# Optimization experiments

Hardware: AMD Instinct MI355X
Metric: run time of the kernel (lower is better)

Reference implementation:

```python
import jax, jax.numpy as jnp
import numpy as np

N_NODES = 50000
N_EDGES = 800000
IN_FEATS = 64
HID_FEATS = 64


def _sage_conv(x, src, dst, W_self, W_neigh, b):
    # mean aggregation over in-neighbors (messages flow src -> dst)
    msg_sum = jax.ops.segment_sum(x[src], dst, num_segments=N_NODES)  # [N, d]
    deg = jax.ops.segment_sum(jnp.ones((src.shape[0],), x.dtype), dst,
                              num_segments=N_NODES)  # [N]
    h_neigh = msg_sum / jnp.maximum(deg, 1.0)[:, None]  # zero-degree nodes -> 0
    return x @ W_self + h_neigh @ W_neigh + b


def setup_inputs() -> dict:
    key = jax.random.key(0)
    ks = jax.random.split(key, 12)
    inputs = jax.random.normal(ks[0], (N_NODES, IN_FEATS), dtype=jnp.float32)
    src = jax.random.randint(ks[1], (N_EDGES,), 0, N_NODES, dtype=jnp.int32)
    dst = jax.random.randint(ks[2], (N_EDGES,), 0, N_NODES, dtype=jnp.int32)

    def glorot(k, shape):
        lim = float(np.sqrt(6.0 / (shape[0] + shape[1])))
        return jax.random.uniform(k, shape, jnp.float32, -lim, lim)

    return {
        "inputs": inputs, "src": src, "dst": dst,
        "W_self1": glorot(ks[3], (IN_FEATS, HID_FEATS)),
        "W_neigh1": glorot(ks[4], (IN_FEATS, HID_FEATS)),
        "b1": jnp.zeros((HID_FEATS,), jnp.float32),
        "W_self2": glorot(ks[5], (HID_FEATS, HID_FEATS)),
        "W_neigh2": glorot(ks[6], (HID_FEATS, HID_FEATS)),
        "b2": jnp.zeros((HID_FEATS,), jnp.float32),
        "W_self3": glorot(ks[7], (HID_FEATS, 1)),
        "W_neigh3": glorot(ks[8], (HID_FEATS, 1)),
        "b3": jnp.zeros((1,), jnp.float32),
    }


def reference(inputs, src, dst,
              W_self1, W_neigh1, b1,
              W_self2, W_neigh2, b2,
              W_self3, W_neigh3, b3):
    h = jax.nn.relu(_sage_conv(inputs, src, dst, W_self1, W_neigh1, b1))
    h = jax.nn.relu(_sage_conv(h, src, dst, W_self2, W_neigh2, b2))
    h = _sage_conv(h, src, dst, W_self3, W_neigh3, b3)
    return h  # [N_NODES, 1]
```

## Files before the change

kernel.cpp:

```cpp
#include <hip/hip_runtime.h>

#define N_NODES 50000
#define N_EDGES 800000
#define F 64
#define NTILES (N_NODES / 16)

#define BNODES 128
#define NB ((N_NODES + BNODES - 1) / BNODES)
#define BCAP 2560
#define EPB 3200
#define SCAT_BLOCKS (N_EDGES / EPB)
#define PREP_ELEMS (4 * F * F + N_NODES * 16)
#define PREP_BLOCKS ((PREP_ELEMS + 511) / 512)

typedef __attribute__((ext_vector_type(8))) short short8;
typedef __attribute__((ext_vector_type(4))) float f32x4;

union frag16 { uint4 u; short8 s; };


__device__ __forceinline__ float bflo(unsigned int u) {
    union { unsigned int i; float f; } c; c.i = u << 16; return c.f;
}
__device__ __forceinline__ float bfhi(unsigned int u) {
    union { unsigned int i; float f; } c; c.i = u & 0xFFFF0000u; return c.f;
}
__device__ __forceinline__ unsigned short f2bf(float f) {
    union { float f; unsigned int i; } c; c.f = f;
    unsigned int r = c.i + 0x7FFF + ((c.i >> 16) & 1);
    return (unsigned short)(r >> 16);
}


__global__ __launch_bounds__(512) void scatter_prep(
        const int* __restrict__ src, const int* __restrict__ dst,
        int* __restrict__ bcur, unsigned int* __restrict__ binned,
        const float* __restrict__ W0, const float* __restrict__ W1,
        const float* __restrict__ W2, const float* __restrict__ W3,
        unsigned short* __restrict__ Wt,
        const float4* __restrict__ xin, ushort4* __restrict__ xout) {
    if (blockIdx.x >= SCAT_BLOCKS) {
        int idx = (blockIdx.x - SCAT_BLOCKS) * 512 + threadIdx.x;
        if (idx < 4 * F * F) {
            int m = idx >> 12;
            int e = idx & 4095;
            int n = e >> 6, k = e & 63;
            const float* W = (m == 0) ? W0 : (m == 1) ? W1 : (m == 2) ? W2 : W3;
            Wt[m * F * F + n * F + k] = f2bf(W[k * F + n]);
            return;
        }
        int i = idx - 4 * F * F;
        if (i >= N_NODES * 16) return;
        float4 v = xin[i];
        ushort4 o;
        o.x = f2bf(v.x); o.y = f2bf(v.y); o.z = f2bf(v.z); o.w = f2bf(v.w);
        xout[i] = o;
        return;
    }

    __shared__ int lcnt[NB];
    __shared__ int scan[512];
    __shared__ int gbase[NB];
    __shared__ int lcur[NB];
    __shared__ unsigned int staged[EPB];
    int tid = threadIdx.x;
    int e0 = blockIdx.x * EPB;
    int e1 = min(N_EDGES, e0 + EPB);
    for (int i = tid; i < NB; i += 512) lcnt[i] = 0;
    __syncthreads();
    for (int i = e0 + tid; i < e1; i += 512)
        atomicAdd(&lcnt[dst[i] >> 7], 1);
    __syncthreads();
    int v = (tid < NB) ? lcnt[tid] : 0;
    scan[tid] = v;
    __syncthreads();
    for (int off = 1; off < 512; off <<= 1) {
        int t = (tid >= off) ? scan[tid - off] : 0;
        __syncthreads();
        scan[tid] += t;
        __syncthreads();
    }
    if (tid < NB) {
        int excl = scan[tid] - v;
        int resv = (v > 0) ? atomicAdd(&bcur[tid], v) : 0;
        gbase[tid] = tid * BCAP + resv - excl;
        lcur[tid] = excl;
    }
    __syncthreads();
    for (int i = e0 + tid; i < e1; i += 512) {
        int d = dst[i];
        int b = d >> 7;
        int dl = d & 127;
        int posl = atomicAdd(&lcur[b], 1);
        staged[posl] = (unsigned)src[i] | ((unsigned)dl << 16) | ((unsigned)b << 23);
    }
    __syncthreads();
    int cnt = e1 - e0;
    for (int i = tid; i < cnt; i += 512) {
        unsigned pk = staged[i];
        int b = pk >> 23;
        binned[gbase[b] + i] = pk;
    }
}


__global__ __launch_bounds__(256) void bucket_build(const unsigned int* __restrict__ binned,
                                                    const int* __restrict__ bcur,
                                                    int* __restrict__ row_beg,
                                                    unsigned short* __restrict__ degs,
                                                    unsigned short* __restrict__ csr16) {
    int b = blockIdx.x;
    int start = b * BCAP;
    int cnt = bcur[b];
    __shared__ int ncnt[BNODES];
    __shared__ int nofs[BNODES];
    __shared__ int ncur[BNODES];
    int tid = threadIdx.x;
    for (int i = tid; i < BNODES; i += 256) ncnt[i] = 0;
    __syncthreads();
    for (int i = tid; i < cnt; i += 256)
        atomicAdd(&ncnt[(binned[start + i] >> 16) & 127], 1);
    __syncthreads();
    if (tid < 128) nofs[tid] = ncnt[tid];
    __syncthreads();
    for (int off = 1; off < 128; off <<= 1) {
        int t = (tid >= off && tid < 128) ? nofs[tid - off] : 0;
        __syncthreads();
        if (tid < 128) nofs[tid] += t;
        __syncthreads();
    }
    if (tid < 128) {
        int excl = nofs[tid] - ncnt[tid];
        ncur[tid] = excl;
        int node = b * BNODES + tid;
        row_beg[node] = start + excl;
        degs[node] = (unsigned short)ncnt[tid];
    }
    __syncthreads();
    for (int i = tid; i < cnt; i += 256) {
        unsigned pk = binned[start + i];
        int dl = (pk >> 16) & 127;
        int pos = start + atomicAdd(&ncur[dl], 1);
        csr16[pos] = (unsigned short)(pk & 0xFFFF);
    }
}


__global__ __launch_bounds__(256) void aggregate_kernel(
        const uint4* __restrict__ xh8, const int* __restrict__ row_beg,
        const unsigned short* __restrict__ degs,
        const unsigned short* __restrict__ csr16, uint4* __restrict__ aggh8, int n_nodes) {
    int wave = threadIdx.x >> 6;
    int lane = threadIdx.x & 63;
    int node = blockIdx.x * 4 + wave;
    if (node >= n_nodes) return;
    int g   = lane >> 3;
    int sub = lane & 7;
    int beg = row_beg[node];
    int deg = degs[node];
    int end = beg + deg;
    float a0[8], a1[8];
    #pragma unroll
    for (int j = 0; j < 8; ++j) { a0[j] = 0.f; a1[j] = 0.f; }
    int i = beg + g;
    for (; i + 8 < end; i += 16) {
        int i0 = csr16[i];
        int i1 = csr16[i + 8];
        uint4 v0 = xh8[i0 * 8 + sub];
        uint4 v1 = xh8[i1 * 8 + sub];
        a0[0] += bflo(v0.x); a0[1] += bfhi(v0.x); a0[2] += bflo(v0.y); a0[3] += bfhi(v0.y);
        a0[4] += bflo(v0.z); a0[5] += bfhi(v0.z); a0[6] += bflo(v0.w); a0[7] += bfhi(v0.w);
        a1[0] += bflo(v1.x); a1[1] += bfhi(v1.x); a1[2] += bflo(v1.y); a1[3] += bfhi(v1.y);
        a1[4] += bflo(v1.z); a1[5] += bfhi(v1.z); a1[6] += bflo(v1.w); a1[7] += bfhi(v1.w);
    }
    if (i < end) {
        uint4 v0 = xh8[csr16[i] * 8 + sub];
        a0[0] += bflo(v0.x); a0[1] += bfhi(v0.x); a0[2] += bflo(v0.y); a0[3] += bfhi(v0.y);
        a0[4] += bflo(v0.z); a0[5] += bfhi(v0.z); a0[6] += bflo(v0.w); a0[7] += bfhi(v0.w);
    }
    float s[8];
    #pragma unroll
    for (int j = 0; j < 8; ++j) s[j] = a0[j] + a1[j];
    #pragma unroll
    for (int off = 8; off <= 32; off <<= 1)
        #pragma unroll
        for (int j = 0; j < 8; ++j)
            s[j] += __shfl_xor(s[j], off);
    if (g == 0) {
        float inv = (deg > 0) ? (1.0f / (float)deg) : 0.f;
        unsigned short o[8];
        #pragma unroll
        for (int j = 0; j < 8; ++j) o[j] = f2bf(s[j] * inv);
        uint4 pk;
        pk.x = (unsigned)o[0] | ((unsigned)o[1] << 16);
        pk.y = (unsigned)o[2] | ((unsigned)o[3] << 16);
        pk.z = (unsigned)o[4] | ((unsigned)o[5] << 16);
        pk.w = (unsigned)o[6] | ((unsigned)o[7] << 16);
        aggh8[node * 8 + sub] = pk;
    }
}


__global__ __launch_bounds__(256) void mfma_transform(
        const uint4* __restrict__ xh, const uint4* __restrict__ aggh,
        const uint4* __restrict__ Wst, const uint4* __restrict__ Wnt,
        const float* __restrict__ b,
        unsigned short* __restrict__ out_bf,
        const float* __restrict__ Ws3, const float* __restrict__ Wn3,
        float* __restrict__ pout, float* __restrict__ qout, int ntiles) {
    int wv   = threadIdx.x >> 6;
    int lane = threadIdx.x & 63;
    int tile = blockIdx.x * 4 + wv;
    if (tile >= ntiles) return;
    int lo = lane & 15, hi = lane >> 4;

    frag16 ws[2][4], wn[2][4];
    #pragma unroll
    for (int kt = 0; kt < 2; ++kt)
        #pragma unroll
        for (int jt = 0; jt < 4; ++jt) {
            int n = jt * 16 + lo;
            ws[kt][jt].u = Wst[n * 8 + kt * 4 + hi];
            wn[kt][jt].u = Wnt[n * 8 + kt * 4 + hi];
        }

    float bias_s[4];
    #pragma unroll
    for (int jt = 0; jt < 4; ++jt) bias_s[jt] = b[jt * 16 + lo];
    float w3n_s[4], w3s_s[4];
    if (pout) {
        #pragma unroll
        for (int jt = 0; jt < 4; ++jt) {
            w3n_s[jt] = Wn3[jt * 16 + lo];
            w3s_s[jt] = Ws3[jt * 16 + lo];
        }
    }

    int base = tile * 16;
    int node = base + lo;

    frag16 ax[2], aa[2];
    #pragma unroll
    for (int kt = 0; kt < 2; ++kt) {
        ax[kt].u = xh[node * 8 + kt * 4 + hi];
        aa[kt].u = aggh[node * 8 + kt * 4 + hi];
    }

    f32x4 acc[4];
    #pragma unroll
    for (int jt = 0; jt < 4; ++jt)
        acc[jt] = f32x4{bias_s[jt], bias_s[jt], bias_s[jt], bias_s[jt]};

    #pragma unroll
    for (int kt = 0; kt < 2; ++kt)
        #pragma unroll
        for (int jt = 0; jt < 4; ++jt) {
            acc[jt] = __builtin_amdgcn_mfma_f32_16x16x32_bf16(ax[kt].s, ws[kt][jt].s, acc[jt], 0, 0, 0);
            acc[jt] = __builtin_amdgcn_mfma_f32_16x16x32_bf16(aa[kt].s, wn[kt][jt].s, acc[jt], 0, 0, 0);
        }

    if (out_bf) {
        #pragma unroll
        for (int jt = 0; jt < 4; ++jt)
            #pragma unroll
            for (int r = 0; r < 4; ++r) {
                float h = fmaxf(acc[jt][r], 0.f);
                out_bf[(base + hi * 4 + r) * F + jt * 16 + lo] = f2bf(h);
            }
    } else {
        #pragma unroll
        for (int r = 0; r < 4; ++r) {
            float pr = 0.f, qr = 0.f;
            #pragma unroll
            for (int jt = 0; jt < 4; ++jt) {
                float h = fmaxf(acc[jt][r], 0.f);
                pr += h * w3n_s[jt];
                qr += h * w3s_s[jt];
            }
            #pragma unroll
            for (int off = 1; off < 16; off <<= 1) {
                pr += __shfl_xor(pr, off);
                qr += __shfl_xor(qr, off);
            }
            if (lo == 0) {
                pout[base + hi * 4 + r] = pr;
                qout[base + hi * 4 + r] = qr;
            }
        }
    }
}


__global__ __launch_bounds__(256) void final_kernel(
        const int* __restrict__ row_beg, const unsigned short* __restrict__ degs,
        const unsigned short* __restrict__ csr16,
        const float* __restrict__ p, const float* __restrict__ q,
        const float* __restrict__ b3, float* __restrict__ out, int n_nodes) {
    int grp = threadIdx.x >> 4;
    int ln  = threadIdx.x & 15;
    int node = blockIdx.x * 16 + grp;
    if (node >= n_nodes) return;
    int beg = row_beg[node];
    int deg = degs[node];
    int end = beg + deg;
    float s = 0.f;
    for (int i = beg + ln; i < end; i += 16) s += p[csr16[i]];
    #pragma unroll
    for (int off = 1; off < 16; off <<= 1) s += __shfl_xor(s, off);
    if (ln == 0) {
        float inv = (deg > 0) ? (1.0f / (float)deg) : 0.f;
        out[node] = q[node] + s * inv + b3[0];
    }
}


extern "C" void kernel_launch(void* const* d_in, const int* in_sizes, int n_in,
                              void* d_out, int out_size, void* d_ws, size_t ws_size,
                              hipStream_t stream) {
    const float* x   = (const float*)d_in[0];
    const int*   src = (const int*)d_in[1];
    const int*   dst = (const int*)d_in[2];
    const float* Ws1 = (const float*)d_in[3];
    const float* Wn1 = (const float*)d_in[4];
    const float* b1  = (const float*)d_in[5];
    const float* Ws2 = (const float*)d_in[6];
    const float* Wn2 = (const float*)d_in[7];
    const float* b2  = (const float*)d_in[8];
    const float* Ws3 = (const float*)d_in[9];
    const float* Wn3 = (const float*)d_in[10];
    const float* b3  = (const float*)d_in[11];
    float* out = (float*)d_out;

    char* ws = (char*)d_ws;
    size_t cur = 0;
    auto alloc = [&](size_t bytes) -> void* {
        void* p = ws + cur;
        cur += (bytes + 255) & ~(size_t)255;
        return p;
    };

    int*            bcur     = (int*)  alloc(NB * sizeof(int));
    unsigned int*   binned   = (unsigned int*)alloc((size_t)NB * BCAP * sizeof(unsigned int));
    int*            row_beg  = (int*)  alloc((size_t)(NB * BNODES) * sizeof(int));
    unsigned short* degs     = (unsigned short*)alloc((size_t)(NB * BNODES) * sizeof(unsigned short));
    unsigned short* csr16    = (unsigned short*)alloc((size_t)NB * BCAP * sizeof(unsigned short));
    unsigned short* xh       = (unsigned short*)alloc((size_t)N_NODES * F * 2);
    unsigned short* h1h      = (unsigned short*)alloc((size_t)N_NODES * F * 2);
    unsigned short* aggh     = (unsigned short*)alloc((size_t)N_NODES * F * 2);
    unsigned short* Wt       = (unsigned short*)alloc(4 * F * F * 2);
    float*          p        = (float*)alloc(N_NODES * sizeof(float));
    float*          q        = (float*)alloc(N_NODES * sizeof(float));

    unsigned short* Wst1 = Wt;
    unsigned short* Wnt1 = Wt + F * F;
    unsigned short* Wst2 = Wt + 2 * F * F;
    unsigned short* Wnt2 = Wt + 3 * F * F;

    (void)hipMemsetAsync(bcur, 0, NB * sizeof(int), stream);
    scatter_prep<<<SCAT_BLOCKS + PREP_BLOCKS, 512, 0, stream>>>(
        src, dst, bcur, binned,
        Ws1, Wn1, Ws2, Wn2, Wt, (const float4*)x, (ushort4*)xh);
    bucket_build<<<NB, 256, 0, stream>>>(binned, bcur, row_beg, degs, csr16);

    int agg_grid = (N_NODES + 3) / 4;
    int tf_grid  = (NTILES + 3) / 4;

    aggregate_kernel<<<agg_grid, 256, 0, stream>>>(
        (const uint4*)xh, row_beg, degs, csr16, (uint4*)aggh, N_NODES);
    mfma_transform<<<tf_grid, 256, 0, stream>>>(
        (const uint4*)xh, (const uint4*)aggh, (const uint4*)Wst1, (const uint4*)Wnt1,
        b1, h1h, nullptr, nullptr, nullptr, nullptr, NTILES);
    aggregate_kernel<<<agg_grid, 256, 0, stream>>>(
        (const uint4*)h1h, row_beg, degs, csr16, (uint4*)aggh, N_NODES);
    mfma_transform<<<tf_grid, 256, 0, stream>>>(
        (const uint4*)h1h, (const uint4*)aggh, (const uint4*)Wst2, (const uint4*)Wnt2,
        b2, nullptr, Ws3, Wn3, p, q, NTILES);
    final_kernel<<<(N_NODES + 15) / 16, 256, 0, stream>>>(
        row_beg, degs, csr16, p, q, b3, out, N_NODES);
}
```

Measured before the change: 182.0 us.

## Fuse all GNN stages into one cooperative persistent kernel with grid syncs

Replaces the seven separate kernel launches (scatter, bucket build, two aggregate/transform pairs, final) with a single cooperative persistent kernel of 512 blocks that runs each phase in grid-stride loops and separates them with grid.sync(). Edge loads in scatter and bucket phases are now held in registers instead of being re-read, and EPB shrinks so the edge chunks fit within the fixed grid. The aim is to remove launch gaps and inter-kernel tail effects. In exchange, each phase is limited to a fixed grid and pays grid-wide barrier costs. A non-cooperative multi-kernel fallback is used if the cooperative launch fails.

```diff
diff --git a/kernel.cpp b/kernel.cpp
--- a/kernel.cpp
+++ b/kernel.cpp
@@ -1,4 +1,7 @@
 #include <hip/hip_runtime.h>
+#include <hip/hip_cooperative_groups.h>
+
+namespace cg = cooperative_groups;
 
 #define N_NODES 50000
 #define N_EDGES 800000
@@ -8,10 +11,13 @@
 #define BNODES 128
 #define NB ((N_NODES + BNODES - 1) / BNODES)
 #define BCAP 2560
-#define EPB 3200
-#define SCAT_BLOCKS (N_EDGES / EPB)
+#define EPB 2048
+#define SCHUNKS ((N_EDGES + EPB - 1) / EPB)
+#define GRID 512
+#define BLOCK 512
+#define NWAVES (GRID * BLOCK / 64)
+#define NGRP16 (GRID * BLOCK / 16)
 #define PREP_ELEMS (4 * F * F + N_NODES * 16)
-#define PREP_BLOCKS ((PREP_ELEMS + 511) / 512)
 
 typedef __attribute__((ext_vector_type(8))) short short8;
 typedef __attribute__((ext_vector_type(4))) float f32x4;
@@ -32,186 +38,222 @@
 }
 
 
-__global__ __launch_bounds__(512) void scatter_prep(
+union SMem {
+    struct {
+        int lcnt[NB];
+        int scan[BLOCK];
+        int gbase[NB];
+        int lcur[NB];
+        unsigned int staged[EPB];
+    } sc;
+    struct {
+        int ncnt[BNODES];
+        int nofs[BNODES];
+        int ncur[BNODES];
+    } bk;
+};
+
+
+__device__ void phase_scatter_prep(
         const int* __restrict__ src, const int* __restrict__ dst,
         int* __restrict__ bcur, unsigned int* __restrict__ binned,
         const float* __restrict__ W0, const float* __restrict__ W1,
         const float* __restrict__ W2, const float* __restrict__ W3,
         unsigned short* __restrict__ Wt,
-        const float4* __restrict__ xin, ushort4* __restrict__ xout) {
-    if (blockIdx.x >= SCAT_BLOCKS) {
-        int idx = (blockIdx.x - SCAT_BLOCKS) * 512 + threadIdx.x;
+        const float4* __restrict__ xin, ushort4* __restrict__ xout,
+        SMem& sm) {
+    int tid = threadIdx.x;
+    int blk = blockIdx.x;
+
+    for (int idx = blk * BLOCK + tid; idx < PREP_ELEMS; idx += GRID * BLOCK) {
         if (idx < 4 * F * F) {
             int m = idx >> 12;
             int e = idx & 4095;
             int n = e >> 6, k = e & 63;
             const float* W = (m == 0) ? W0 : (m == 1) ? W1 : (m == 2) ? W2 : W3;
             Wt[m * F * F + n * F + k] = f2bf(W[k * F + n]);
-            return;
-        }
-        int i = idx - 4 * F * F;
-        if (i >= N_NODES * 16) return;
-        float4 v = xin[i];
-        ushort4 o;
-        o.x = f2bf(v.x); o.y = f2bf(v.y); o.z = f2bf(v.z); o.w = f2bf(v.w);
-        xout[i] = o;
-        return;
-    }
-
-    __shared__ int lcnt[NB];
-    __shared__ int scan[512];
-    __shared__ int gbase[NB];
-    __shared__ int lcur[NB];
-    __shared__ unsigned int staged[EPB];
+        } else {
+            int i = idx - 4 * F * F;
+            float4 v = xin[i];
+            ushort4 o;
+            o.x = f2bf(v.x); o.y = f2bf(v.y); o.z = f2bf(v.z); o.w = f2bf(v.w);
+            xout[i] = o;
+        }
+    }
+
+    if (blk >= SCHUNKS) return;
+
+    int e0 = blk * EPB;
+    int e1 = min(N_EDGES, e0 + EPB);
+    for (int i = tid; i < NB; i += BLOCK) sm.sc.lcnt[i] = 0;
+    __syncthreads();
+
+    int dreg[4], sreg[4];
+    #pragma unroll
+    for (int t = 0; t < 4; ++t) {
+        int i = e0 + tid + t * BLOCK;
+        if (i < e1) { dreg[t] = dst[i]; sreg[t] = src[i]; }
+        else        { dreg[t] = -1;     sreg[t] = 0; }
+    }
+    #pragma unroll
+    for (int t = 0; t < 4; ++t)
+        if (dreg[t] >= 0) atomicAdd(&sm.sc.lcnt[dreg[t] >> 7], 1);
+    __syncthreads();
+
+    int v = (tid < NB) ? sm.sc.lcnt[tid] : 0;
+    sm.sc.scan[tid] = v;
+    __syncthreads();
+    for (int off = 1; off < BLOCK; off <<= 1) {
+        int t2 = (tid >= off) ? sm.sc.scan[tid - off] : 0;
+        __syncthreads();
+        sm.sc.scan[tid] += t2;
+        __syncthreads();
+    }
+    if (tid < NB) {
+        int excl = sm.sc.scan[tid] - v;
+        int resv = (v > 0) ? atomicAdd(&bcur[tid], v) : 0;
+        sm.sc.gbase[tid] = tid * BCAP + resv - excl;
+        sm.sc.lcur[tid] = excl;
+    }
+    __syncthreads();
+
+    #pragma unroll
+    for (int t = 0; t < 4; ++t) {
+        if (dreg[t] >= 0) {
+            int d = dreg[t];
+            int b = d >> 7;
+            int dl = d & 127;
+            int posl = atomicAdd(&sm.sc.lcur[b], 1);
+            sm.sc.staged[posl] =
+                (unsigned)sreg[t] | ((unsigned)dl << 16) | ((unsigned)b << 23);
+        }
+    }
+    __syncthreads();
+
+    int cnt = e1 - e0;
+    for (int i = tid; i < cnt; i += BLOCK) {
+        unsigned pk = sm.sc.staged[i];
+        binned[sm.sc.gbase[pk >> 23] + i] = pk;
+    }
+}
+
+
+__device__ void phase_bucket(
+        const unsigned int* __restrict__ binned, const int* __restrict__ bcur,
+        int* __restrict__ row_beg, unsigned short* __restrict__ degs,
+        unsigned short* __restrict__ csr16, SMem& sm) {
+    int blk = blockIdx.x;
+    if (blk >= NB) return;
     int tid = threadIdx.x;
-    int e0 = blockIdx.x * EPB;
-    int e1 = min(N_EDGES, e0 + EPB);
-    for (int i = tid; i < NB; i += 512) lcnt[i] = 0;
-    __syncthreads();
-    for (int i = e0 + tid; i < e1; i += 512)
-        atomicAdd(&lcnt[dst[i] >> 7], 1);
-    __syncthreads();
-    int v = (tid < NB) ? lcnt[tid] : 0;
-    scan[tid] = v;
-    __syncthreads();
-    for (int off = 1; off < 512; off <<= 1) {
-        int t = (tid >= off) ? scan[tid - off] : 0;
+    int start = blk * BCAP;
+    int cnt = min(bcur[blk], BCAP);
+
+    for (int i = tid; i < BNODES; i += BLOCK) sm.bk.ncnt[i] = 0;
+    __syncthreads();
+
+    unsigned preg[5];
+    #pragma unroll
+    for (int t = 0; t < 5; ++t) {
+        int i = tid + t * BLOCK;
+        preg[t] = (i < cnt) ? binned[start + i] : 0xFFFFFFFFu;
+    }
+    #pragma unroll
+    for (int t = 0; t < 5; ++t)
+        if (preg[t] != 0xFFFFFFFFu)
+            atomicAdd(&sm.bk.ncnt[(preg[t] >> 16) & 127], 1);
+    __syncthreads();
+
+    if (tid < BNODES) sm.bk.nofs[tid] = sm.bk.ncnt[tid];
+    __syncthreads();
+    for (int off = 1; off < BNODES; off <<= 1) {
+        int t2 = (tid >= off && tid < BNODES) ? sm.bk.nofs[tid - off] : 0;
         __syncthreads();
-        scan[tid] += t;
+        if (tid < BNODES) sm.bk.nofs[tid] += t2;
         __syncthreads();
     }
-    if (tid < NB) {
-        int excl = scan[tid] - v;
-        int resv = (v > 0) ? atomicAdd(&bcur[tid], v) : 0;
-        gbase[tid] = tid * BCAP + resv - excl;
-        lcur[tid] = excl;
-    }
-    __syncthreads();
-    for (int i = e0 + tid; i < e1; i += 512) {
-        int d = dst[i];
-        int b = d >> 7;
-        int dl = d & 127;
-        int posl = atomicAdd(&lcur[b], 1);
-        staged[posl] = (unsigned)src[i] | ((unsigned)dl << 16) | ((unsigned)b << 23);
-    }
-    __syncthreads();
-    int cnt = e1 - e0;
-    for (int i = tid; i < cnt; i += 512) {
-        unsigned pk = staged[i];
-        int b = pk >> 23;
-        binned[gbase[b] + i] = pk;
-    }
-}
-
-
-__global__ __launch_bounds__(256) void bucket_build(const unsigned int* __restrict__ binned,
-                                                    const int* __restrict__ bcur,
-                                                    int* __restrict__ row_beg,
-                                                    unsigned short* __restrict__ degs,
-                                                    unsigned short* __restrict__ csr16) {
-    int b = blockIdx.x;
-    int start = b * BCAP;
-    int cnt = bcur[b];
-    __shared__ int ncnt[BNODES];
-    __shared__ int nofs[BNODES];
-    __shared__ int ncur[BNODES];
-    int tid = threadIdx.x;
-    for (int i = tid; i < BNODES; i += 256) ncnt[i] = 0;
-    __syncthreads();
-    for (int i = tid; i < cnt; i += 256)
-        atomicAdd(&ncnt[(binned[start + i] >> 16) & 127], 1);
-    __syncthreads();
-    if (tid < 128) nofs[tid] = ncnt[tid];
-    __syncthreads();
-    for (int off = 1; off < 128; off <<= 1) {
-        int t = (tid >= off && tid < 128) ? nofs[tid - off] : 0;
-        __syncthreads();
-        if (tid < 128) nofs[tid] += t;
-        __syncthreads();
-    }
-    if (tid < 128) {
-        int excl = nofs[tid] - ncnt[tid];
-        ncur[tid] = excl;
-        int node = b * BNODES + tid;
+    if (tid < BNODES) {
+        int excl = sm.bk.nofs[tid] - sm.bk.ncnt[tid];
+        sm.bk.ncur[tid] = excl;
+        int node = blk * BNODES + tid;
         row_beg[node] = start + excl;
-        degs[node] = (unsigned short)ncnt[tid];
-    }
-    __syncthreads();
-    for (int i = tid; i < cnt; i += 256) {
-        unsigned pk = binned[start + i];
-        int dl = (pk >> 16) & 127;
-        int pos = start + atomicAdd(&ncur[dl], 1);
-        csr16[pos] = (unsigned short)(pk & 0xFFFF);
-    }
-}
-
-
-__global__ __launch_bounds__(256) void aggregate_kernel(
+        degs[node] = (unsigned short)sm.bk.ncnt[tid];
+    }
+    __syncthreads();
+
+    #pragma unroll
+    for (int t = 0; t < 5; ++t) {
+        if (preg[t] != 0xFFFFFFFFu) {
+            unsigned pk = preg[t];
+            int dl = (pk >> 16) & 127;
+            int pos = start + atomicAdd(&sm.bk.ncur[dl], 1);
+            csr16[pos] = (unsigned short)(pk & 0xFFFF);
+        }
+    }
+}
+
+
+__device__ void aggregate_phase(
         const uint4* __restrict__ xh8, const int* __restrict__ row_beg,
         const unsigned short* __restrict__ degs,
-        const unsigned short* __restrict__ csr16, uint4* __restrict__ aggh8, int n_nodes) {
-    int wave = threadIdx.x >> 6;
-    int lane = threadIdx.x & 63;
-    int node = blockIdx.x * 4 + wave;
-    if (node >= n_nodes) return;
+        const unsigned short* __restrict__ csr16, uint4* __restrict__ aggh8,
+        int gwave, int lane) {
     int g   = lane >> 3;
     int sub = lane & 7;
-    int beg = row_beg[node];
-    int deg = degs[node];
-    int end = beg + deg;
-    float a0[8], a1[8];
-    #pragma unroll
-    for (int j = 0; j < 8; ++j) { a0[j] = 0.f; a1[j] = 0.f; }
-    int i = beg + g;
-    for (; i + 8 < end; i += 16) {
-        int i0 = csr16[i];
-        int i1 = csr16[i + 8];
-        uint4 v0 = xh8[i0 * 8 + sub];
-        uint4 v1 = xh8[i1 * 8 + sub];
-        a0[0] += bflo(v0.x); a0[1] += bfhi(v0.x); a0[2] += bflo(v0.y); a0[3] += bfhi(v0.y);
-        a0[4] += bflo(v0.z); a0[5] += bfhi(v0.z); a0[6] += bflo(v0.w); a0[7] += bfhi(v0.w);
-        a1[0] += bflo(v1.x); a1[1] += bfhi(v1.x); a1[2] += bflo(v1.y); a1[3] += bfhi(v1.y);
-        a1[4] += bflo(v1.z); a1[5] += bfhi(v1.z); a1[6] += bflo(v1.w); a1[7] += bfhi(v1.w);
-    }
-    if (i < end) {
-        uint4 v0 = xh8[csr16[i] * 8 + sub];
-        a0[0] += bflo(v0.x); a0[1] += bfhi(v0.x); a0[2] += bflo(v0.y); a0[3] += bfhi(v0.y);
-        a0[4] += bflo(v0.z); a0[5] += bfhi(v0.z); a0[6] += bflo(v0.w); a0[7] += bfhi(v0.w);
-    }
-    float s[8];
-    #pragma unroll
-    for (int j = 0; j < 8; ++j) s[j] = a0[j] + a1[j];
-    #pragma unroll
-    for (int off = 8; off <= 32; off <<= 1)
-        #pragma unroll
-        for (int j = 0; j < 8; ++j)
-            s[j] += __shfl_xor(s[j], off);
-    if (g == 0) {
-        float inv = (deg > 0) ? (1.0f / (float)deg) : 0.f;
-        unsigned short o[8];
-        #pragma unroll
-        for (int j = 0; j < 8; ++j) o[j] = f2bf(s[j] * inv);
-        uint4 pk;
-        pk.x = (unsigned)o[0] | ((unsigned)o[1] << 16);
-        pk.y = (unsigned)o[2] | ((unsigned)o[3] << 16);
-        pk.z = (unsigned)o[4] | ((unsigned)o[5] << 16);
-        pk.w = (unsigned)o[6] | ((unsigned)o[7] << 16);
-        aggh8[node * 8 + sub] = pk;
-    }
-}
-
-
-__global__ __launch_bounds__(256) void mfma_transform(
+    for (int node = gwave; node < N_NODES; node += NWAVES) {
+        int beg = row_beg[node];
+        int deg = degs[node];
+        int end = beg + deg;
+        float a0[8], a1[8];
+        #pragma unroll
+        for (int j = 0; j < 8; ++j) { a0[j] = 0.f; a1[j] = 0.f; }
+        int i = beg + g;
+        for (; i + 8 < end; i += 16) {
+            int i0 = csr16[i];
+            int i1 = csr16[i + 8];
+            uint4 v0 = xh8[i0 * 8 + sub];
+            uint4 v1 = xh8[i1 * 8 + sub];
+            a0[0] += bflo(v0.x); a0[1] += bfhi(v0.x); a0[2] += bflo(v0.y); a0[3] += bfhi(v0.y);
+            a0[4] += bflo(v0.z); a0[5] += bfhi(v0.z); a0[6] += bflo(v0.w); a0[7] += bfhi(v0.w);
+            a1[0] += bflo(v1.x); a1[1] += bfhi(v1.x); a1[2] += bflo(v1.y); a1[3] += bfhi(v1.y);
+            a1[4] += bflo(v1.z); a1[5] += bfhi(v1.z); a1[6] += bflo(v1.w); a1[7] += bfhi(v1.w);
+        }
+        if (i < end) {
+            uint4 v0 = xh8[csr16[i] * 8 + sub];
+            a0[0] += bflo(v0.x); a0[1] += bfhi(v0.x); a0[2] += bflo(v0.y); a0[3] += bfhi(v0.y);
+            a0[4] += bflo(v0.z); a0[5] += bfhi(v0.z); a0[6] += bflo(v0.w); a0[7] += bfhi(v0.w);
+        }
+        float s[8];
+        #pragma unroll
+        for (int j = 0; j < 8; ++j) s[j] = a0[j] + a1[j];
+        #pragma unroll
+        for (int off = 8; off <= 32; off <<= 1)
+            #pragma unroll
+            for (int j = 0; j < 8; ++j)
+                s[j] += __shfl_xor(s[j], off);
+        if (g == 0) {
+            float inv = (deg > 0) ? (1.0f / (float)deg) : 0.f;
+            unsigned short o[8];
+            #pragma unroll
+            for (int j = 0; j < 8; ++j) o[j] = f2bf(s[j] * inv);
+            uint4 pk;
+            pk.x = (unsigned)o[0] | ((unsigned)o[1] << 16);
+            pk.y = (unsigned)o[2] | ((unsigned)o[3] << 16);
+            pk.z = (unsigned)o[4] | ((unsigned)o[5] << 16);
+            pk.w = (unsigned)o[6] | ((unsigned)o[7] << 16);
+            aggh8[node * 8 + sub] = pk;
+        }
+    }
+}
+
+
+template <bool PROJ>
+__device__ void transform_phase(
         const uint4* __restrict__ xh, const uint4* __restrict__ aggh,
         const uint4* __restrict__ Wst, const uint4* __restrict__ Wnt,
-        const float* __restrict__ b,
-        unsigned short* __restrict__ out_bf,
+        const float* __restrict__ b, unsigned short* __restrict__ out_bf,
         const float* __restrict__ Ws3, const float* __restrict__ Wn3,
-        float* __restrict__ pout, float* __restrict__ qout, int ntiles) {
-    int wv   = threadIdx.x >> 6;
-    int lane = threadIdx.x & 63;
-    int tile = blockIdx.x * 4 + wv;
-    if (tile >= ntiles) return;
+        float* __restrict__ pout, float* __restrict__ qout,
+        int gwave, int lane) {
     int lo = lane & 15, hi = lane >> 4;
 
     frag16 ws[2][4], wn[2][4];
@@ -223,12 +265,11 @@
             ws[kt][jt].u = Wst[n * 8 + kt * 4 + hi];
             wn[kt][jt].u = Wnt[n * 8 + kt * 4 + hi];
         }
-
     float bias_s[4];
     #pragma unroll
     for (int jt = 0; jt < 4; ++jt) bias_s[jt] = b[jt * 16 + lo];
     float w3n_s[4], w3s_s[4];
-    if (pout) {
+    if constexpr (PROJ) {
         #pragma unroll
         for (int jt = 0; jt < 4; ++jt) {
             w3n_s[jt] = Wn3[jt * 16 + lo];
@@ -236,81 +277,170 @@
         }
     }
 
-    int base = tile * 16;
-    int node = base + lo;
-
-    frag16 ax[2], aa[2];
-    #pragma unroll
-    for (int kt = 0; kt < 2; ++kt) {
-        ax[kt].u = xh[node * 8 + kt * 4 + hi];
-        aa[kt].u = aggh[node * 8 + kt * 4 + hi];
-    }
-
-    f32x4 acc[4];
-    #pragma unroll
-    for (int jt = 0; jt < 4; ++jt)
-        acc[jt] = f32x4{bias_s[jt], bias_s[jt], bias_s[jt], bias_s[jt]};
-
-    #pragma unroll
-    for (int kt = 0; kt < 2; ++kt)
-        #pragma unroll
-        for (int jt = 0; jt < 4; ++jt) {
-            acc[jt] = __builtin_amdgcn_mfma_f32_16x16x32_bf16(ax[kt].s, ws[kt][jt].s, acc[jt], 0, 0, 0);
-            acc[jt] = __builtin_amdgcn_mfma_f32_16x16x32_bf16(aa[kt].s, wn[kt][jt].s, acc[jt], 0, 0, 0);
-        }
-
-    if (out_bf) {
+    for (int tile = gwave; tile < NTILES; tile += NWAVES) {
+        int base = tile * 16;
+        int node = base + lo;
+
+        frag16 ax[2], aa[2];
+        #pragma unroll
+        for (int kt = 0; kt < 2; ++kt) {
+            ax[kt].u = xh[node * 8 + kt * 4 + hi];
+            aa[kt].u = aggh[node * 8 + kt * 4 + hi];
+        }
+
+        f32x4 acc[4];
         #pragma unroll
         for (int jt = 0; jt < 4; ++jt)
+            acc[jt] = f32x4{bias_s[jt], bias_s[jt], bias_s[jt], bias_s[jt]};
+
+        #pragma unroll
+        for (int kt = 0; kt < 2; ++kt)
+            #pragma unroll
+            for (int jt = 0; jt < 4; ++jt) {
+                acc[jt] = __builtin_amdgcn_mfma_f32_16x16x32_bf16(ax[kt].s, ws[kt][jt].s, acc[jt], 0, 0, 0);
+                acc[jt] = __builtin_amdgcn_mfma_f32_16x16x32_bf16(aa[kt].s, wn[kt][jt].s, acc[jt], 0, 0, 0);
+            }
+
+        if constexpr (!PROJ) {
+            #pragma unroll
+            for (int jt = 0; jt < 4; ++jt)
+                #pragma unroll
+                for (int r = 0; r < 4; ++r) {
+                    float h = fmaxf(acc[jt][r], 0.f);
+                    out_bf[(base + hi * 4 + r) * F + jt * 16 + lo] = f2bf(h);
+                }
+        } else {
             #pragma unroll
             for (int r = 0; r < 4; ++r) {
-                float h = fmaxf(acc[jt][r], 0.f);
-                out_bf[(base + hi * 4 + r) * F + jt * 16 + lo] = f2bf(h);
+                float pr = 0.f, qr = 0.f;
+                #pragma unroll
+                for (int jt = 0; jt < 4; ++jt) {
+                    float h = fmaxf(acc[jt][r], 0.f);
+                    pr += h * w3n_s[jt];
+                    qr += h * w3s_s[jt];
+                }
+                #pragma unroll
+                for (int off = 1; off < 16; off <<= 1) {
+                    pr += __shfl_xor(pr, off);
+                    qr += __shfl_xor(qr, off);
+                }
+                if (lo == 0) {
+                    pout[base + hi * 4 + r] = pr;
+                    qout[base + hi * 4 + r] = qr;
+                }
             }
-    } else {
-        #pragma unroll
-        for (int r = 0; r < 4; ++r) {
-            float pr = 0.f, qr = 0.f;
-            #pragma unroll
-            for (int jt = 0; jt < 4; ++jt) {
-                float h = fmaxf(acc[jt][r], 0.f);
-                pr += h * w3n_s[jt];
-                qr += h * w3s_s[jt];
-            }
-            #pragma unroll
-            for (int off = 1; off < 16; off <<= 1) {
-                pr += __shfl_xor(pr, off);
-                qr += __shfl_xor(qr, off);
-            }
-            if (lo == 0) {
-                pout[base + hi * 4 + r] = pr;
-                qout[base + hi * 4 + r] = qr;
-            }
-        }
-    }
-}
-
-
-__global__ __launch_bounds__(256) void final_kernel(
+        }
+    }
+}
+
+
+__device__ void final_phase(
         const int* __restrict__ row_beg, const unsigned short* __restrict__ degs,
         const unsigned short* __restrict__ csr16,
         const float* __restrict__ p, const float* __restrict__ q,
-        const float* __restrict__ b3, float* __restrict__ out, int n_nodes) {
-    int grp = threadIdx.x >> 4;
-    int ln  = threadIdx.x & 15;
-    int node = blockIdx.x * 16 + grp;
-    if (node >= n_nodes) return;
-    int beg = row_beg[node];
-    int deg = degs[node];
-    int end = beg + deg;
-    float s = 0.f;
-    for (int i = beg + ln; i < end; i += 16) s += p[csr16[i]];
-    #pragma unroll
-    for (int off = 1; off < 16; off <<= 1) s += __shfl_xor(s, off);
-    if (ln == 0) {
-        float inv = (deg > 0) ? (1.0f / (float)deg) : 0.f;
-        out[node] = q[node] + s * inv + b3[0];
-    }
+        const float* __restrict__ b3, float* __restrict__ out,
+        int blk, int tid) {
+    int ggrp = (blk * BLOCK + tid) >> 4;
+    int ln = tid & 15;
+    for (int node = ggrp; node < N_NODES; node += NGRP16) {
+        int beg = row_beg[node];
+        int deg = degs[node];
+        int end = beg + deg;
+        float s = 0.f;
+        for (int i = beg + ln; i < end; i += 16) s += p[csr16[i]];
+        #pragma unroll
+        for (int off = 1; off < 16; off <<= 1) s += __shfl_xor(s, off);
+        if (ln == 0) {
+            float inv = (deg > 0) ? (1.0f / (float)deg) : 0.f;
+            out[node] = q[node] + s * inv + b3[0];
+        }
+    }
+}
+
+
+__global__ __launch_bounds__(BLOCK, 4) void fused_all(
+        const float* __restrict__ x, const int* __restrict__ src,
+        const int* __restrict__ dst,
+        const float* __restrict__ W0, const float* __restrict__ W1,
+        const float* __restrict__ W2, const float* __restrict__ W3,
+        const float* __restrict__ b1, const float* __restrict__ b2,
+        const float* __restrict__ Ws3, const float* __restrict__ Wn3,
+        const float* __restrict__ b3,
+        int* __restrict__ bcur, unsigned int* __restrict__ binned,
+        int* __restrict__ row_beg, unsigned short* __restrict__ degs,
+        unsigned short* __restrict__ csr16, unsigned short* __restrict__ xh,
+        unsigned short* __restrict__ h1h, unsigned short* __restrict__ aggh,
+        unsigned short* __restrict__ Wt, float* __restrict__ p,
+        float* __restrict__ q, float* __restrict__ out) {
+    cg::grid_group grid = cg::this_grid();
+    __shared__ SMem sm;
+    int tid = threadIdx.x;
+    int lane = tid & 63;
+    int gwave = (blockIdx.x * BLOCK + tid) >> 6;
+
+    phase_scatter_prep(src, dst, bcur, binned, W0, W1, W2, W3, Wt,
+                       (const float4*)x, (ushort4*)xh, sm);
+    grid.sync();
+    phase_bucket(binned, bcur, row_beg, degs, csr16, sm);
+    grid.sync();
+    aggregate_phase((const uint4*)xh, row_beg, degs, csr16, (uint4*)aggh, gwave, lane);
+    grid.sync();
+    transform_phase<false>((const uint4*)xh, (const uint4*)aggh,
+                           (const uint4*)Wt, (const uint4*)(Wt + F * F), b1,
+                           h1h, nullptr, nullptr, nullptr, nullptr, gwave, lane);
+    grid.sync();
+    aggregate_phase((const uint4*)h1h, row_beg, degs, csr16, (uint4*)aggh, gwave, lane);
+    grid.sync();
+    transform_phase<true>((const uint4*)h1h, (const uint4*)aggh,
+                          (const uint4*)(Wt + 2 * F * F), (const uint4*)(Wt + 3 * F * F), b2,
+                          nullptr, Ws3, Wn3, p, q, gwave, lane);
+    grid.sync();
+    final_phase(row_beg, degs, csr16, p, q, b3, out, blockIdx.x, tid);
+}
+
+
+__global__ __launch_bounds__(BLOCK, 4) void k_scatter_prep(
+        const int* src, const int* dst, int* bcur, unsigned int* binned,
+        const float* W0, const float* W1, const float* W2, const float* W3,
+        unsigned short* Wt, const float4* xin, ushort4* xout) {
+    __shared__ SMem sm;
+    phase_scatter_prep(src, dst, bcur, binned, W0, W1, W2, W3, Wt, xin, xout, sm);
+}
+
+__global__ __launch_bounds__(BLOCK, 4) void k_bucket(
+        const unsigned int* binned, const int* bcur, int* row_beg,
+        unsigned short* degs, unsigned short* csr16) {
+    __shared__ SMem sm;
+    phase_bucket(binned, bcur, row_beg, degs, csr16, sm);
+}
+
+__global__ __launch_bounds__(BLOCK, 4) void k_aggregate(
+        const uint4* xh8, const int* row_beg, const unsigned short* degs,
+        const unsigned short* csr16, uint4* aggh8) {
+    int gwave = (blockIdx.x * BLOCK + threadIdx.x) >> 6;
+    aggregate_phase(xh8, row_beg, degs, csr16, aggh8, gwave, threadIdx.x & 63);
+}
+
+__global__ __launch_bounds__(BLOCK, 4) void k_tf_mid(
+        const uint4* xh, const uint4* aggh, const uint4* Wst, const uint4* Wnt,
+        const float* b, unsigned short* out_bf) {
+    int gwave = (blockIdx.x * BLOCK + threadIdx.x) >> 6;
+    transform_phase<false>(xh, aggh, Wst, Wnt, b, out_bf,
+                           nullptr, nullptr, nullptr, nullptr, gwave, threadIdx.x & 63);
+}
+
+__global__ __launch_bounds__(BLOCK, 4) void k_tf_last(
+        const uint4* xh, const uint4* aggh, const uint4* Wst, const uint4* Wnt,
+        const float* b, const float* Ws3, const float* Wn3, float* p, float* q) {
+    int gwave = (blockIdx.x * BLOCK + threadIdx.x) >> 6;
+    transform_phase<true>(xh, aggh, Wst, Wnt, b, nullptr,
+                          Ws3, Wn3, p, q, gwave, threadIdx.x & 63);
+}
+
+__global__ __launch_bounds__(BLOCK, 4) void k_final(
+        const int* row_beg, const unsigned short* degs, const unsigned short* csr16,
+        const float* p, const float* q, const float* b3, float* out) {
+    final_phase(row_beg, degs, csr16, p, q, b3, out, blockIdx.x, threadIdx.x);
 }
 
 
@@ -334,9 +464,9 @@
     char* ws = (char*)d_ws;
     size_t cur = 0;
     auto alloc = [&](size_t bytes) -> void* {
-        void* p = ws + cur;
+        void* ptr = ws + cur;
         cur += (bytes + 255) & ~(size_t)255;
-        return p;
+        return ptr;
     };
 
     int*            bcur     = (int*)  alloc(NB * sizeof(int));
@@ -351,30 +481,35 @@
     float*          p        = (float*)alloc(N_NODES * sizeof(float));
     float*          q        = (float*)alloc(N_NODES * sizeof(float));
 
-    unsigned short* Wst1 = Wt;
-    unsigned short* Wnt1 = Wt + F * F;
-    unsigned short* Wst2 = Wt + 2 * F * F;
-    unsigned short* Wnt2 = Wt + 3 * F * F;
-
     (void)hipMemsetAsync(bcur, 0, NB * sizeof(int), stream);
-    scatter_prep<<<SCAT_BLOCKS + PREP_BLOCKS, 512, 0, stream>>>(
-        src, dst, bcur, binned,
-        Ws1, Wn1, Ws2, Wn2, Wt, (const float4*)x, (ushort4*)xh);
-    bucket_build<<<NB, 256, 0, stream>>>(binned, bcur, row_beg, degs, csr16);
-
-    int agg_grid = (N_NODES + 3) / 4;
-    int tf_grid  = (NTILES + 3) / 4;
-
-    aggregate_kernel<<<agg_grid, 256, 0, stream>>>(
-        (const uint4*)xh, row_beg, degs, csr16, (uint4*)aggh, N_NODES);
-    mfma_transform<<<tf_grid, 256, 0, stream>>>(
-        (const uint4*)xh, (const uint4*)aggh, (const uint4*)Wst1, (const uint4*)Wnt1,
-        b1, h1h, nullptr, nullptr, nullptr, nullptr, NTILES);
-    aggregate_kernel<<<agg_grid, 256, 0, stream>>>(
-        (const uint4*)h1h, row_beg, degs, csr16, (uint4*)aggh, N_NODES);
-    mfma_transform<<<tf_grid, 256, 0, stream>>>(
-        (const uint4*)h1h, (const uint4*)aggh, (const uint4*)Wst2, (const uint4*)Wnt2,
-        b2, nullptr, Ws3, Wn3, p, q, NTILES);
-    final_kernel<<<(N_NODES + 15) / 16, 256, 0, stream>>>(
-        row_beg, degs, csr16, p, q, b3, out, N_NODES);
-}
+
+    void* ka[] = {
+        (void*)&x, (void*)&src, (void*)&dst,
+        (void*)&Ws1, (void*)&Wn1, (void*)&Ws2, (void*)&Wn2,
+        (void*)&b1, (void*)&b2, (void*)&Ws3, (void*)&Wn3, (void*)&b3,
+        (void*)&bcur, (void*)&binned, (void*)&row_beg, (void*)&degs,
+        (void*)&csr16, (void*)&xh, (void*)&h1h, (void*)&aggh,
+        (void*)&Wt, (void*)&p, (void*)&q, (void*)&out
+    };
+    hipError_t err = hipLaunchCooperativeKernel(
+        (void*)fused_all, dim3(GRID), dim3(BLOCK), ka, 0, stream);
+
+    if (err != hipSuccess) {
+        k_scatter_prep<<<GRID, BLOCK, 0, stream>>>(
+            src, dst, bcur, binned, Ws1, Wn1, Ws2, Wn2, Wt,
+            (const float4*)x, (ushort4*)xh);
+        k_bucket<<<NB, BLOCK, 0, stream>>>(binned, bcur, row_beg, degs, csr16);
+        k_aggregate<<<GRID, BLOCK, 0, stream>>>(
+            (const uint4*)xh, row_beg, degs, csr16, (uint4*)aggh);
+        k_tf_mid<<<GRID, BLOCK, 0, stream>>>(
+            (const uint4*)xh, (const uint4*)aggh,
+            (const uint4*)Wt, (const uint4*)(Wt + F * F), b1, h1h);
+        k_aggregate<<<GRID, BLOCK, 0, stream>>>(
+            (const uint4*)h1h, row_beg, degs, csr16, (uint4*)aggh);
+        k_tf_last<<<GRID, BLOCK, 0, stream>>>(
+            (const uint4*)h1h, (const uint4*)aggh,
+            (const uint4*)(Wt + 2 * F * F), (const uint4*)(Wt + 3 * F * F), b2,
+            Ws3, Wn3, p, q);
+        k_final<<<GRID, BLOCK, 0, stream>>>(row_beg, degs, csr16, p, q, b3, out);
+    }
+}
```

After: 576.0 us. 3.17x slower.
